# Optimization experiments

Measured on AMD Instinct MI355X. Metric: run time of the kernel, lower is better.

Reference implementation:

```python
import jax, jax.numpy as jnp
import numpy as np

NBINS = (128, 64, 32)
LOG2PI = float(np.log(2.0 * np.pi))


def _quadratic_spline_stack(x, genes_oi, local_gene_ix, delta, uh, uw):
    """Stack of piecewise-quadratic (piecewise-linear density) splines on [0,1].
    Per split with n heights / n-1 widths (n-1 bins). Returns (outputs, logabsdet)."""
    uh_oi = uh[genes_oi]  # [G, sum(n)]
    uw_oi = uw[genes_oi]  # [G, sum(n-1)]
    outputs = x
    logabsdet = jnp.zeros_like(x)
    oh = ow = od = 0
    for n in NBINS:
        nh, nw = n, n - 1
        uhs = uh_oi[:, oh:oh + nh]
        uws = uw_oi[:, ow:ow + nw]
        ds = delta[:, od:od + nh]
        oh += nh; ow += nw; od += nh
        # per-gene bin widths / locations
        widths_g = jax.nn.softmax(uws, axis=-1)                     # [G, nw]
        bl = jnp.cumsum(widths_g, axis=-1)
        bl = bl.at[:, -1].set(1.0)
        bin_loc_g = jnp.pad(bl, ((0, 0), (1, 0)))                   # [G, nw+1]
        # gather per cut
        w = widths_g[local_gene_ix]                                 # [N, nw]
        loc = bin_loc_g[local_gene_ix]                              # [N, nw+1]
        # per-cut knot heights: gene baseline + cell/gene delta, normalized to unit area
        h_un = jnp.exp(uhs[local_gene_ix] + ds)                     # [N, nh]
        area = jnp.sum(0.5 * (h_un[:, :-1] + h_un[:, 1:]) * w, axis=-1, keepdims=True)
        h = h_un / area                                             # [N, nh]
        seg = 0.5 * (h[:, :-1] + h[:, 1:]) * w                      # bin masses [N, nw]
        left_cdf = jnp.pad(jnp.cumsum(seg, axis=-1)[:, :-1], ((0, 0), (1, 0)))  # [N, nw]
        # locate bin
        bin_idx = jnp.clip(jnp.sum(outputs[:, None] >= loc, axis=-1) - 1, 0, nw - 1)
        gi = bin_idx[:, None]
        loc_l = jnp.take_along_axis(loc, gi, -1)[:, 0]
        w_b = jnp.take_along_axis(w, gi, -1)[:, 0]
        cdf_l = jnp.take_along_axis(left_cdf, gi, -1)[:, 0]
        h_l = jnp.take_along_axis(h, gi, -1)[:, 0]
        h_r = jnp.take_along_axis(h, gi + 1, -1)[:, 0]
        alpha = (outputs - loc_l) / w_b
        outputs = (0.5 * (h_r - h_l) * w_b) * alpha * alpha + h_l * w_b * alpha + cdf_l
        logabsdet = logabsdet + jnp.log(h_l + (h_r - h_l) * alpha)
    return outputs, logabsdet


def setup_inputs() -> dict:
    key = jax.random.key(0)
    ks = jax.random.split(key, 10)
    B, L, G_total, G_oi, C, N = 512, 16, 20000, 500, 224, 200000
    clustering = jax.random.uniform(ks[0], (B, L), dtype=jnp.float32)
    coordinates = jax.random.uniform(ks[1], (N,), dtype=jnp.float32, minval=1e-4, maxval=1.0 - 1e-4)
    genes_oi = jax.random.randint(ks[2], (G_oi,), 0, G_total)
    local_gene_ix = jax.random.randint(ks[3], (N,), 0, G_oi)
    local_cellxgene_ix = jax.random.randint(ks[4], (N,), 0, B * G_oi)
    localcellxgene_ix = jax.random.randint(ks[5], (N,), 0, B * G_total)
    logit_weight = jax.random.normal(ks[6], (G_total, L, C), dtype=jnp.float32) * 0.01
    rho_weight = jax.random.normal(ks[7], (G_total, L), dtype=jnp.float32) * 0.05
    rho_bias = 1e-5 + (1.0 - 1e-5) * jax.random.uniform(ks[8], (G_total,), dtype=jnp.float32)
    k9, k10 = jax.random.split(ks[9])
    unnormalized_heights = jax.random.normal(k9, (G_total, sum(NBINS)), dtype=jnp.float32) * 0.1
    unnormalized_widths = jax.random.normal(k10, (G_total, sum(n - 1 for n in NBINS)), dtype=jnp.float32) * 0.1
    return dict(clustering=clustering, coordinates=coordinates, genes_oi=genes_oi,
                local_gene_ix=local_gene_ix, local_cellxgene_ix=local_cellxgene_ix,
                localcellxgene_ix=localcellxgene_ix, logit_weight=logit_weight,
                rho_weight=rho_weight, rho_bias=rho_bias,
                unnormalized_heights=unnormalized_heights,
                unnormalized_widths=unnormalized_widths)


def reference(clustering, coordinates, genes_oi, local_gene_ix, local_cellxgene_ix,
              localcellxgene_ix, logit_weight, rho_weight, rho_bias,
              unnormalized_heights, unnormalized_widths):
    B = clustering.shape[0]
    G = genes_oi.shape[0]
    n_total_genes = rho_bias.shape[0]
    # Decoder (n_layers=0 -> nn_output = latent)
    lw_oi = logit_weight[genes_oi]                                   # [G, L, C]
    mixture_delta = jnp.einsum('bl,glc->bgc', clustering, lw_oi)     # [B, G, C]
    rho_delta = clustering @ rho_weight.T                            # [B, G_total]
    rho = jax.nn.softmax(jnp.log(rho_bias)[None, :] + rho_delta, axis=-1)
    rho_cuts = rho.reshape(-1)[localcellxgene_ix]                    # [N]
    md_cuts = mixture_delta.reshape(B * G, -1)[local_cellxgene_ix]   # [N, C]
    _, lik_mixture = _quadratic_spline_stack(coordinates, genes_oi, local_gene_ix,
                                             md_cuts, unnormalized_heights, unnormalized_widths)
    lik_overall = jnp.log(rho_cuts) + jnp.log(jnp.float32(n_total_genes))
    elbo = -jnp.sum(lik_mixture + lik_overall)
    # Normal(0, exp(log_scale=0)=1) regularization log-probs
    def normal_logpdf(v):
        return -0.5 * v * v - 0.5 * LOG2PI
    elbo = elbo - jnp.sum(normal_logpdf(lw_oi))
    elbo = elbo - jnp.sum(normal_logpdf(rho_weight[genes_oi]))
    return elbo
```

## Files before the change

### kernel.cpp

```cpp
#include <hip/hip_runtime.h>
#include <cstddef>

#define LOG2PI_F 1.8378770664093453f

__device__ __forceinline__ float wave_sum(float v) {
#pragma unroll
    for (int o = 32; o >= 1; o >>= 1) v += __shfl_xor(v, o, 64);
    return v;
}
__device__ __forceinline__ float wave_max(float v) {
#pragma unroll
    for (int o = 32; o >= 1; o >>= 1) v = fmaxf(v, __shfl_xor(v, o, 64));
    return v;
}
__device__ __forceinline__ float wave_scan_incl(float v, int lane) {
#pragma unroll
    for (int o = 1; o < 64; o <<= 1) {
        float t = __shfl_up(v, o, 64);
        if (lane >= o) v += t;
    }
    return v;
}

__global__ void k_logrb(const float* __restrict__ rho_bias, float* __restrict__ logrb, int G_total) {
    int g = blockIdx.x * blockDim.x + threadIdx.x;
    if (g < G_total) logrb[g] = __logf(rho_bias[g]);
}

__global__ void k_prep_genes(const int* __restrict__ genes_oi,
                             const float* __restrict__ uh, const float* __restrict__ uw,
                             float4* __restrict__ pk) {
    const int g = blockIdx.x;
    const int t = threadIdx.x;
    const int gs = genes_oi[g];
    const float* uhg = uh + (size_t)gs * 224;
    const float* uwg = uw + (size_t)gs * 221;
    float4* pkg = pk + (size_t)g * 224;

    const int NH[3] = {128, 64, 32};
    const int OH[3] = {0, 128, 192};
    const int OW[3] = {0, 127, 190};
    const int SO[3] = {0, 128, 191};
#pragma unroll
    for (int lev = 0; lev < 3; ++lev) {
        const int nw = NH[lev] - 1;
        float v0 = (t < nw)      ? uwg[OW[lev] + t]      : -INFINITY;
        float v1 = (t + 64 < nw) ? uwg[OW[lev] + t + 64] : -INFINITY;
        float mx = wave_max(fmaxf(v0, v1));
        float e0 = (t < nw)      ? __expf(v0 - mx) : 0.f;
        float e1 = (t + 64 < nw) ? __expf(v1 - mx) : 0.f;
        float inv = 1.0f / wave_sum(e0 + e1);
        float w0 = e0 * inv, w1 = e1 * inv;
        float i0 = wave_scan_incl(w0, t);
        float tot0 = __shfl(i0, 63, 64);
        float i1 = wave_scan_incl(w1, t) + tot0;
        if (t < nw) {
            float loc = (t == nw - 1) ? 1.0f : i0;
            pkg[SO[lev] + t] = make_float4(uhg[OH[lev] + t + 1], 0.5f * w0, loc, 0.f);
        }
        if (t + 64 < nw) {
            int j = t + 64;
            float loc = (j == nw - 1) ? 1.0f : i1;
            pkg[SO[lev] + j] = make_float4(uhg[OH[lev] + j + 1], 0.5f * w1, loc, 0.f);
        }
    }
    if (t == 0) pkg[127] = make_float4(uhg[0], uhg[128], uhg[192], 0.f);
}

__global__ void k_prep_lwT(const int* __restrict__ genes_oi,
                           const float* __restrict__ lw, const float* __restrict__ rw,
                           float* __restrict__ lwT, float* __restrict__ pB) {
    const int g = blockIdx.x;
    const int tid = threadIdx.x;
    const int gs = genes_oi[g];
    const float* src = lw + (size_t)gs * 3584;
    float* dst = lwT + (size_t)g * 3584;
    float acc = 0.f;
    if (tid < 224) {
        float vv[16];
#pragma unroll
        for (int l = 0; l < 16; ++l) {
            float v = src[l * 224 + tid];
            vv[l] = v;
            acc = fmaf(v, v, acc);
        }
        float4* d4 = (float4*)(dst + (size_t)tid * 16);
#pragma unroll
        for (int q = 0; q < 4; ++q)
            d4[q] = make_float4(vv[4 * q + 0], vv[4 * q + 1], vv[4 * q + 2], vv[4 * q + 3]);
    }
    if (tid < 16) { float v = rw[(size_t)gs * 16 + tid]; acc = fmaf(v, v, acc); }
    __shared__ float sm[256];
    sm[tid] = acc;
    __syncthreads();
    for (int o = 128; o > 0; o >>= 1) { if (tid < o) sm[tid] += sm[tid + o]; __syncthreads(); }
    if (tid == 0) pB[g] = 0.5f * sm[0] + 0.5f * LOG2PI_F * (3584.0f + 16.0f);
}

__global__ void k_lse(const float* __restrict__ clustering, const float* __restrict__ rw,
                      const float* __restrict__ logrb, float* __restrict__ lse, int G_total) {
    const int b = blockIdx.x;
    const int tid = threadIdx.x;
    __shared__ float cl_s[16];
    if (tid < 16) cl_s[tid] = clustering[(size_t)b * 16 + tid];
    __syncthreads();
    float m = -INFINITY, s = 0.f;
    for (int g = tid; g < G_total; g += blockDim.x) {
        const float4* r4 = (const float4*)(rw + (size_t)g * 16);
        float d = 0.f;
#pragma unroll
        for (int q = 0; q < 4; ++q) {
            float4 v = r4[q];
            d = fmaf(cl_s[4 * q + 0], v.x, d);
            d = fmaf(cl_s[4 * q + 1], v.y, d);
            d = fmaf(cl_s[4 * q + 2], v.z, d);
            d = fmaf(cl_s[4 * q + 3], v.w, d);
        }
        float logit = logrb[g] + d;
        float mn = fmaxf(m, logit);
        s = s * __expf(m - mn) + __expf(logit - mn);
        m = mn;
    }
    __shared__ float ms[256], ss[256];
    ms[tid] = m; ss[tid] = s;
    __syncthreads();
    for (int o = 128; o > 0; o >>= 1) {
        if (tid < o) {
            float m2 = ms[tid + o], s2 = ss[tid + o];
            float mn = fmaxf(ms[tid], m2);
            ss[tid] = ss[tid] * __expf(ms[tid] - mn) + s2 * __expf(m2 - mn);
            ms[tid] = mn;
        }
        __syncthreads();
    }
    if (tid == 0) lse[b] = ms[0] + __logf(ss[0]);
}

__global__ void k_zero(int* __restrict__ p, int n) {
    int i = blockIdx.x * blockDim.x + threadIdx.x;
    if (i < n) p[i] = 0;
}

__global__ void k_hist(const int* __restrict__ lcx, int* __restrict__ counts, int N, int G_oi) {
    int i = blockIdx.x * blockDim.x + threadIdx.x;
    if (i < N) atomicAdd(&counts[(unsigned)lcx[i] % (unsigned)G_oi], 1);
}

__global__ void k_scan(const int* __restrict__ counts, int* __restrict__ offsets,
                       int* __restrict__ cursor, int G_oi) {
    __shared__ int sm[512];
    const int t = threadIdx.x;
    int v = (t < G_oi) ? counts[t] : 0;
    sm[t] = v;
    __syncthreads();
    for (int o = 1; o < 512; o <<= 1) {
        int add = (t >= o) ? sm[t - o] : 0;
        __syncthreads();
        sm[t] += add;
        __syncthreads();
    }
    if (t < G_oi) {
        offsets[t + 1] = sm[t];
        cursor[t] = sm[t] - v;
    }
    if (t == 0) offsets[0] = 0;
}

__global__ void k_scatter(const float* __restrict__ coord, const int* __restrict__ lgix,
                          const int* __restrict__ lcx, const int* __restrict__ lc2,
                          int* __restrict__ cursor,
                          float* __restrict__ xs, int* __restrict__ b1s,
                          int* __restrict__ lc2s, int* __restrict__ ghs, int N, int G_oi) {
    int i = blockIdx.x * blockDim.x + threadIdx.x;
    if (i >= N) return;
    unsigned v = (unsigned)lcx[i];
    unsigned g = v % (unsigned)G_oi;
    int pos = atomicAdd(&cursor[g], 1);
    xs[pos]   = coord[i];
    b1s[pos]  = (int)(v / (unsigned)G_oi);
    lc2s[pos] = lc2[i];
    ghs[pos]  = lgix[i];
}

__launch_bounds__(512, 4)
__global__ void k_main2(const float* __restrict__ xs, const int* __restrict__ b1s,
                        const int* __restrict__ lc2s, const int* __restrict__ ghs,
                        const int* __restrict__ offsets,
                        const float* __restrict__ clustering,
                        const float* __restrict__ lwT,
                        const float4* __restrict__ pk,
                        const float* __restrict__ rw,
                        const float* __restrict__ logrb,
                        const float* __restrict__ lse,
                        float* __restrict__ pA, int G_oi, int G_total) {
    const int g = blockIdx.x;
    const int tid = threadIdx.x;
    const float* lwg = lwT + (size_t)g * 3584;
    const int s = offsets[g], e = offsets[g + 1];
    const float logGt = __logf((float)G_total);
    float acc = 0.f;

    for (int base = s; base < e; base += 512) {
        const int i = base + tid;
        const bool valid = i < e;
        const int isafe = valid ? i : s;
        float x = xs[isafe];
        const int b1  = b1s[isafe];
        const int lc2 = lc2s[isafe];
        const int gh  = ghs[isafe];
        const float4* pkh = pk + (size_t)gh * 224;

        float cl[16];
        {
            const float4* c4 = (const float4*)(clustering + (size_t)b1 * 16);
#pragma unroll
            for (int q = 0; q < 4; ++q) {
                float4 v = c4[q];
                cl[4 * q + 0] = v.x; cl[4 * q + 1] = v.y; cl[4 * q + 2] = v.z; cl[4 * q + 3] = v.w;
            }
        }
        const float4 uh0 = pkh[127];
        const float uh0v[3] = {uh0.x, uh0.y, uh0.z};

        float lad = 0.f;
        const int NH[3] = {128, 64, 32};
        const int OH[3] = {0, 128, 192};
        const int SO[3] = {0, 128, 191};
#pragma unroll
        for (int lev = 0; lev < 3; ++lev) {
            const int nw = NH[lev] - 1;
            const float* rowbase = lwg + (size_t)OH[lev] * 16;
            float hp;
            {
                float d = 0.f;
#pragma unroll
                for (int l = 0; l < 16; ++l) d = fmaf(cl[l], rowbase[l], d);
                hp = __expf(uh0v[lev] + d);
            }
            float h_l = hp, h_r = hp, whb = 0.f, loc_l = 0.f, cdf = 0.f, area = 0.f;
            int in = 0;
            const float4* pks = pkh + SO[lev];
            for (int j = 0; j < nw; ++j) {
                const float* row = rowbase + (size_t)(j + 1) * 16;
                float d = 0.f;
#pragma unroll
                for (int l = 0; l < 16; ++l) d = fmaf(cl[l], row[l], d);
                float4 pkv = pks[j];
                float hn = __expf(pkv.x + d);
                float seg = (hp + hn) * pkv.y;
                bool inJ = (in == j);
                if (inJ) { h_r = hn; whb = pkv.y; }
                bool adv = (x >= pkv.z) && (j < nw - 1);
                if (adv) { cdf += seg; h_l = hn; loc_l = pkv.z; in = j + 1; }
                area += seg;
                hp = hn;
            }
            float inv_area = __builtin_amdgcn_rcpf(area);
            float alpha = (x - loc_l) * 0.5f * __builtin_amdgcn_rcpf(whb);
            float t2 = whb * alpha;
            x = (t2 * fmaf(h_r - h_l, alpha, 2.f * h_l) + cdf) * inv_area;
            lad += __logf(fmaf(h_r - h_l, alpha, h_l)) - __logf(area);
        }

        unsigned b2 = (unsigned)lc2 / (unsigned)G_total;
        unsigned gt = (unsigned)lc2 - b2 * (unsigned)G_total;
        float d2 = 0.f;
        {
            const float4* c24 = (const float4*)(clustering + (size_t)b2 * 16);
            const float4* r4  = (const float4*)(rw + (size_t)gt * 16);
#pragma unroll
            for (int q = 0; q < 4; ++q) {
                float4 a = c24[q], b = r4[q];
                d2 = fmaf(a.x, b.x, d2); d2 = fmaf(a.y, b.y, d2);
                d2 = fmaf(a.z, b.z, d2); d2 = fmaf(a.w, b.w, d2);
            }
        }
        float lik = logrb[gt] + d2 - lse[b2] + logGt;
        if (valid) acc -= (lad + lik);
    }

    acc = wave_sum(acc);
    __shared__ float wsm[8];
    if ((tid & 63) == 0) wsm[tid >> 6] = acc;
    __syncthreads();
    if (tid == 0) {
        float t = 0.f;
#pragma unroll
        for (int w = 0; w < 8; ++w) t += wsm[w];
        pA[g] = t;
    }
}

__global__ void k_final(const float* __restrict__ pA, const float* __restrict__ pB,
                        float* __restrict__ out, int nA, int nB) {
    const int tid = threadIdx.x;
    float acc = 0.f;
    for (int i = tid; i < nA; i += blockDim.x) acc += pA[i];
    for (int i = tid; i < nB; i += blockDim.x) acc += pB[i];
    __shared__ float sm[256];
    sm[tid] = acc;
    __syncthreads();
    for (int o = 128; o > 0; o >>= 1) { if (tid < o) sm[tid] += sm[tid + o]; __syncthreads(); }
    if (tid == 0) out[0] = sm[0];
}

extern "C" void kernel_launch(void* const* d_in, const int* in_sizes, int n_in,
                              void* d_out, int out_size, void* d_ws, size_t ws_size,
                              hipStream_t stream) {
    const float* clustering        = (const float*)d_in[0];
    const float* coordinates       = (const float*)d_in[1];
    const int*   genes_oi          = (const int*)d_in[2];
    const int*   local_gene_ix     = (const int*)d_in[3];
    const int*   local_cellxgene_ix= (const int*)d_in[4];
    const int*   localcellxgene_ix = (const int*)d_in[5];
    const float* lw                = (const float*)d_in[6];
    const float* rw                = (const float*)d_in[7];
    const float* rho_bias          = (const float*)d_in[8];
    const float* uh                = (const float*)d_in[9];
    const float* uw                = (const float*)d_in[10];

    const int G_total = in_sizes[8];
    const int G_oi    = in_sizes[2];
    const int N       = in_sizes[1];
    const int L       = in_sizes[7] / G_total;
    const int B       = in_sizes[0] / L;

    size_t off = 0;
    char* base = (char*)d_ws;
    auto alloc = [&](size_t nbytes) {
        char* p = base + off;
        off = (off + nbytes + 15) & ~(size_t)15;
        return (void*)p;
    };
    float*  pA      = (float*)alloc(sizeof(float) * (G_oi + 16));
    float*  pB      = (float*)alloc(sizeof(float) * (G_oi + 16));
    float*  lse     = (float*)alloc(sizeof(float) * (B + 16));
    float*  logrb   = (float*)alloc(sizeof(float) * G_total);
    float*  lwT     = (float*)alloc(sizeof(float) * (size_t)G_oi * 3584);
    float4* pk      = (float4*)alloc(sizeof(float4) * (size_t)G_oi * 224);
    int*    counts  = (int*)alloc(sizeof(int) * 512);
    int*    offsets = (int*)alloc(sizeof(int) * 512);
    int*    cursor  = (int*)alloc(sizeof(int) * 512);
    float*  xs      = (float*)alloc(sizeof(float) * N);
    int*    b1s     = (int*)alloc(sizeof(int) * N);
    int*    lc2s    = (int*)alloc(sizeof(int) * N);
    int*    ghs     = (int*)alloc(sizeof(int) * N);
    (void)ws_size;

    const int TPB = 256;
    k_logrb<<<(G_total + TPB - 1) / TPB, TPB, 0, stream>>>(rho_bias, logrb, G_total);
    k_prep_genes<<<G_oi, 64, 0, stream>>>(genes_oi, uh, uw, pk);
    k_prep_lwT<<<G_oi, 256, 0, stream>>>(genes_oi, lw, rw, lwT, pB);
    k_lse<<<B, 256, 0, stream>>>(clustering, rw, logrb, lse, G_total);
    k_zero<<<2, 256, 0, stream>>>(counts, 512);
    k_hist<<<(N + TPB - 1) / TPB, TPB, 0, stream>>>(local_cellxgene_ix, counts, N, G_oi);
    k_scan<<<1, 512, 0, stream>>>(counts, offsets, cursor, G_oi);
    k_scatter<<<(N + TPB - 1) / TPB, TPB, 0, stream>>>(coordinates, local_gene_ix,
                                                       local_cellxgene_ix, localcellxgene_ix,
                                                       cursor, xs, b1s, lc2s, ghs, N, G_oi);
    k_main2<<<G_oi, 512, 0, stream>>>(xs, b1s, lc2s, ghs, offsets, clustering, lwT, pk,
                                      rw, logrb, lse, pA, G_oi, G_total);
    k_final<<<1, 256, 0, stream>>>(pA, pB, (float*)d_out, G_oi, G_oi);
}
```

Baseline: 674.8 us.

## Fuse prep kernels, stage weights in LDS, pack scatter, move rho likelihood out of main

```diff
diff --git a/kernel.cpp b/kernel.cpp
--- a/kernel.cpp
+++ b/kernel.cpp
@@ -2,6 +2,7 @@
 #include <cstddef>
 
 #define LOG2PI_F 1.8378770664093453f
+#define LOG2E_F  1.4426950408889634f
 
 __device__ __forceinline__ float wave_sum(float v) {
 #pragma unroll
@@ -22,66 +23,32 @@
     return v;
 }
 
-__global__ void k_logrb(const float* __restrict__ rho_bias, float* __restrict__ logrb, int G_total) {
-    int g = blockIdx.x * blockDim.x + threadIdx.x;
-    if (g < G_total) logrb[g] = __logf(rho_bias[g]);
-}
-
-__global__ void k_prep_genes(const int* __restrict__ genes_oi,
-                             const float* __restrict__ uh, const float* __restrict__ uw,
-                             float4* __restrict__ pk) {
-    const int g = blockIdx.x;
-    const int t = threadIdx.x;
-    const int gs = genes_oi[g];
-    const float* uhg = uh + (size_t)gs * 224;
-    const float* uwg = uw + (size_t)gs * 221;
-    float4* pkg = pk + (size_t)g * 224;
-
-    const int NH[3] = {128, 64, 32};
-    const int OH[3] = {0, 128, 192};
-    const int OW[3] = {0, 127, 190};
-    const int SO[3] = {0, 128, 191};
-#pragma unroll
-    for (int lev = 0; lev < 3; ++lev) {
-        const int nw = NH[lev] - 1;
-        float v0 = (t < nw)      ? uwg[OW[lev] + t]      : -INFINITY;
-        float v1 = (t + 64 < nw) ? uwg[OW[lev] + t + 64] : -INFINITY;
-        float mx = wave_max(fmaxf(v0, v1));
-        float e0 = (t < nw)      ? __expf(v0 - mx) : 0.f;
-        float e1 = (t + 64 < nw) ? __expf(v1 - mx) : 0.f;
-        float inv = 1.0f / wave_sum(e0 + e1);
-        float w0 = e0 * inv, w1 = e1 * inv;
-        float i0 = wave_scan_incl(w0, t);
-        float tot0 = __shfl(i0, 63, 64);
-        float i1 = wave_scan_incl(w1, t) + tot0;
-        if (t < nw) {
-            float loc = (t == nw - 1) ? 1.0f : i0;
-            pkg[SO[lev] + t] = make_float4(uhg[OH[lev] + t + 1], 0.5f * w0, loc, 0.f);
-        }
-        if (t + 64 < nw) {
-            int j = t + 64;
-            float loc = (j == nw - 1) ? 1.0f : i1;
-            pkg[SO[lev] + j] = make_float4(uhg[OH[lev] + j + 1], 0.5f * w1, loc, 0.f);
-        }
-    }
-    if (t == 0) pkg[127] = make_float4(uhg[0], uhg[128], uhg[192], 0.f);
-}
-
-__global__ void k_prep_lwT(const int* __restrict__ genes_oi,
-                           const float* __restrict__ lw, const float* __restrict__ rw,
-                           float* __restrict__ lwT, float* __restrict__ pB) {
+__global__ void k_init(const float* __restrict__ rho_bias, float* __restrict__ logrb,
+                       int* __restrict__ counts, float* __restrict__ pC, int G_total) {
+    int i = blockIdx.x * blockDim.x + threadIdx.x;
+    if (i < G_total) logrb[i] = __logf(rho_bias[i]);
+    if (i < 512) counts[i] = 0;
+    if (i == 512 + 0) pC[0] = 0.f;
+}
+
+__global__ void k_prep(const int* __restrict__ genes_oi,
+                       const float* __restrict__ uh, const float* __restrict__ uw,
+                       const float* __restrict__ lw, const float* __restrict__ rw,
+                       float4* __restrict__ pk, float* __restrict__ lwT,
+                       float* __restrict__ pB) {
     const int g = blockIdx.x;
     const int tid = threadIdx.x;
     const int gs = genes_oi[g];
-    const float* src = lw + (size_t)gs * 3584;
-    float* dst = lwT + (size_t)g * 3584;
+
     float acc = 0.f;
     if (tid < 224) {
+        const float* src = lw + (size_t)gs * 3584;
+        float* dst = lwT + (size_t)g * 3584;
         float vv[16];
 #pragma unroll
         for (int l = 0; l < 16; ++l) {
             float v = src[l * 224 + tid];
-            vv[l] = v;
+            vv[l] = v * LOG2E_F;
             acc = fmaf(v, v, acc);
         }
         float4* d4 = (float4*)(dst + (size_t)tid * 16);
@@ -90,6 +57,43 @@
             d4[q] = make_float4(vv[4 * q + 0], vv[4 * q + 1], vv[4 * q + 2], vv[4 * q + 3]);
     }
     if (tid < 16) { float v = rw[(size_t)gs * 16 + tid]; acc = fmaf(v, v, acc); }
+
+    if (tid < 64) {
+        const int t = tid;
+        const float* uhg = uh + (size_t)gs * 224;
+        const float* uwg = uw + (size_t)gs * 221;
+        float4* pkg = pk + (size_t)g * 224;
+        const int NH[3] = {128, 64, 32};
+        const int OH[3] = {0, 128, 192};
+        const int OW[3] = {0, 127, 190};
+        const int SO[3] = {0, 128, 191};
+#pragma unroll
+        for (int lev = 0; lev < 3; ++lev) {
+            const int nw = NH[lev] - 1;
+            float v0 = (t < nw)      ? uwg[OW[lev] + t]      : -INFINITY;
+            float v1 = (t + 64 < nw) ? uwg[OW[lev] + t + 64] : -INFINITY;
+            float mx = wave_max(fmaxf(v0, v1));
+            float e0 = (t < nw)      ? __expf(v0 - mx) : 0.f;
+            float e1 = (t + 64 < nw) ? __expf(v1 - mx) : 0.f;
+            float inv = 1.0f / wave_sum(e0 + e1);
+            float w0 = e0 * inv, w1 = e1 * inv;
+            float i0 = wave_scan_incl(w0, t);
+            float tot0 = __shfl(i0, 63, 64);
+            float i1 = wave_scan_incl(w1, t) + tot0;
+            if (t < nw) {
+                float loc = (t == nw - 1) ? 1.0f : i0;
+                pkg[SO[lev] + t] = make_float4(uhg[OH[lev] + t + 1] * LOG2E_F, 0.5f * w0, loc, 0.f);
+            }
+            if (t + 64 < nw) {
+                int j = t + 64;
+                float loc = (j == nw - 1) ? 1.0f : i1;
+                pkg[SO[lev] + j] = make_float4(uhg[OH[lev] + j + 1] * LOG2E_F, 0.5f * w1, loc, 0.f);
+            }
+        }
+        if (t == 0)
+            pkg[127] = make_float4(uhg[0] * LOG2E_F, uhg[128] * LOG2E_F, uhg[192] * LOG2E_F, 0.f);
+    }
+
     __shared__ float sm[256];
     sm[tid] = acc;
     __syncthreads();
@@ -136,14 +140,35 @@
     if (tid == 0) lse[b] = ms[0] + __logf(ss[0]);
 }
 
-__global__ void k_zero(int* __restrict__ p, int n) {
-    int i = blockIdx.x * blockDim.x + threadIdx.x;
-    if (i < n) p[i] = 0;
-}
-
-__global__ void k_hist(const int* __restrict__ lcx, int* __restrict__ counts, int N, int G_oi) {
-    int i = blockIdx.x * blockDim.x + threadIdx.x;
-    if (i < N) atomicAdd(&counts[(unsigned)lcx[i] % (unsigned)G_oi], 1);
+__global__ void k_histlik(const int* __restrict__ lcx, const int* __restrict__ lc2,
+                          int* __restrict__ counts,
+                          const float* __restrict__ clustering, const float* __restrict__ rw,
+                          const float* __restrict__ logrb, const float* __restrict__ lse,
+                          float* __restrict__ pC, int N, int G_oi, int G_total, float logGt) {
+    const int i = blockIdx.x * blockDim.x + threadIdx.x;
+    float acc = 0.f;
+    if (i < N) {
+        atomicAdd(&counts[(unsigned)lcx[i] % (unsigned)G_oi], 1);
+        const int v = lc2[i];
+        const unsigned b2 = (unsigned)v / (unsigned)G_total;
+        const unsigned gt = (unsigned)v - b2 * (unsigned)G_total;
+        const float4* c4 = (const float4*)(clustering + (size_t)b2 * 16);
+        const float4* r4 = (const float4*)(rw + (size_t)gt * 16);
+        float d2 = 0.f;
+#pragma unroll
+        for (int q = 0; q < 4; ++q) {
+            float4 a = c4[q], b = r4[q];
+            d2 = fmaf(a.x, b.x, d2); d2 = fmaf(a.y, b.y, d2);
+            d2 = fmaf(a.z, b.z, d2); d2 = fmaf(a.w, b.w, d2);
+        }
+        acc = -(logrb[gt] + d2 - lse[b2] + logGt);
+    }
+    acc = wave_sum(acc);
+    __shared__ float wsm[4];
+    if ((threadIdx.x & 63) == 0) wsm[threadIdx.x >> 6] = acc;
+    __syncthreads();
+    if (threadIdx.x == 0)
+        atomicAdd(pC, wsm[0] + wsm[1] + wsm[2] + wsm[3]);
 }
 
 __global__ void k_scan(const int* __restrict__ counts, int* __restrict__ offsets,
@@ -167,116 +192,104 @@
 }
 
 __global__ void k_scatter(const float* __restrict__ coord, const int* __restrict__ lgix,
-                          const int* __restrict__ lcx, const int* __restrict__ lc2,
-                          int* __restrict__ cursor,
-                          float* __restrict__ xs, int* __restrict__ b1s,
-                          int* __restrict__ lc2s, int* __restrict__ ghs, int N, int G_oi) {
+                          const int* __restrict__ lcx, int* __restrict__ cursor,
+                          int2* __restrict__ packed, int N, int G_oi) {
     int i = blockIdx.x * blockDim.x + threadIdx.x;
     if (i >= N) return;
     unsigned v = (unsigned)lcx[i];
     unsigned g = v % (unsigned)G_oi;
     int pos = atomicAdd(&cursor[g], 1);
-    xs[pos]   = coord[i];
-    b1s[pos]  = (int)(v / (unsigned)G_oi);
-    lc2s[pos] = lc2[i];
-    ghs[pos]  = lgix[i];
-}
-
-__launch_bounds__(512, 4)
-__global__ void k_main2(const float* __restrict__ xs, const int* __restrict__ b1s,
-                        const int* __restrict__ lc2s, const int* __restrict__ ghs,
+    packed[pos] = make_int2(__float_as_int(coord[i]),
+                            (int)(((v / (unsigned)G_oi) << 16) | (unsigned)lgix[i]));
+}
+
+__launch_bounds__(512)
+__global__ void k_main2(const int2* __restrict__ packed,
                         const int* __restrict__ offsets,
                         const float* __restrict__ clustering,
                         const float* __restrict__ lwT,
                         const float4* __restrict__ pk,
-                        const float* __restrict__ rw,
-                        const float* __restrict__ logrb,
-                        const float* __restrict__ lse,
-                        float* __restrict__ pA, int G_oi, int G_total) {
+                        float* __restrict__ pA, int G_oi) {
     const int g = blockIdx.x;
     const int tid = threadIdx.x;
-    const float* lwg = lwT + (size_t)g * 3584;
+    __shared__ float lds_lw[3584];
+    {
+        const float* src = lwT + (size_t)g * 3584;
+        for (int k = tid; k < 3584; k += 512) lds_lw[k] = src[k];
+    }
+    __syncthreads();
     const int s = offsets[g], e = offsets[g + 1];
-    const float logGt = __logf((float)G_total);
     float acc = 0.f;
 
     for (int base = s; base < e; base += 512) {
         const int i = base + tid;
-        const bool valid = i < e;
-        const int isafe = valid ? i : s;
-        float x = xs[isafe];
-        const int b1  = b1s[isafe];
-        const int lc2 = lc2s[isafe];
-        const int gh  = ghs[isafe];
-        const float4* pkh = pk + (size_t)gh * 224;
-
-        float cl[16];
-        {
-            const float4* c4 = (const float4*)(clustering + (size_t)b1 * 16);
-#pragma unroll
-            for (int q = 0; q < 4; ++q) {
-                float4 v = c4[q];
-                cl[4 * q + 0] = v.x; cl[4 * q + 1] = v.y; cl[4 * q + 2] = v.z; cl[4 * q + 3] = v.w;
+        if (i < e) {
+            const int2 p = packed[i];
+            float x = __int_as_float(p.x);
+            const int b1 = (int)((unsigned)p.y >> 16);
+            const int gh = p.y & 0xffff;
+            const float4* pkh = pk + (size_t)gh * 224;
+
+            float cl[16];
+            {
+                const float4* c4 = (const float4*)(clustering + (size_t)b1 * 16);
+#pragma unroll
+                for (int q = 0; q < 4; ++q) {
+                    float4 v = c4[q];
+                    cl[4 * q + 0] = v.x; cl[4 * q + 1] = v.y;
+                    cl[4 * q + 2] = v.z; cl[4 * q + 3] = v.w;
+                }
             }
-        }
-        const float4 uh0 = pkh[127];
-        const float uh0v[3] = {uh0.x, uh0.y, uh0.z};
-
-        float lad = 0.f;
-        const int NH[3] = {128, 64, 32};
-        const int OH[3] = {0, 128, 192};
-        const int SO[3] = {0, 128, 191};
-#pragma unroll
-        for (int lev = 0; lev < 3; ++lev) {
-            const int nw = NH[lev] - 1;
-            const float* rowbase = lwg + (size_t)OH[lev] * 16;
-            float hp;
-            {
-                float d = 0.f;
-#pragma unroll
-                for (int l = 0; l < 16; ++l) d = fmaf(cl[l], rowbase[l], d);
-                hp = __expf(uh0v[lev] + d);
+            const float4 uh0 = pkh[127];
+            const float uh0v[3] = {uh0.x, uh0.y, uh0.z};
+
+            float lad = 0.f;
+            const int NH[3] = {128, 64, 32};
+            const int OH[3] = {0, 128, 192};
+            const int SO[3] = {0, 128, 191};
+#pragma unroll
+            for (int lev = 0; lev < 3; ++lev) {
+                const int nw = NH[lev] - 1;
+                const float* rowbase = lds_lw + (size_t)OH[lev] * 16;
+                float hp;
+                {
+                    const float4* rq = (const float4*)rowbase;
+                    float4 r0 = rq[0], r1 = rq[1], r2 = rq[2], r3 = rq[3];
+                    float d0 = fmaf(cl[3], r0.w, fmaf(cl[2], r0.z, fmaf(cl[1], r0.y, cl[0] * r0.x)));
+                    float d1 = fmaf(cl[7], r1.w, fmaf(cl[6], r1.z, fmaf(cl[5], r1.y, cl[4] * r1.x)));
+                    float d2 = fmaf(cl[11], r2.w, fmaf(cl[10], r2.z, fmaf(cl[9], r2.y, cl[8] * r2.x)));
+                    float d3 = fmaf(cl[15], r3.w, fmaf(cl[14], r3.z, fmaf(cl[13], r3.y, cl[12] * r3.x)));
+                    hp = exp2f(uh0v[lev] + (d0 + d1) + (d2 + d3));
+                }
+                float h_l = hp, h_r = hp, whb = 0.f, loc_l = 0.f, cdf = 0.f, area = 0.f;
+                int in = 0;
+                const float4* pks = pkh + SO[lev];
+                float4 pkv = pks[0];
+                for (int j = 0; j < nw; ++j) {
+                    float4 pknext = pks[j + 1];
+                    const float4* rq = (const float4*)(rowbase + (size_t)(j + 1) * 16);
+                    float4 r0 = rq[0], r1 = rq[1], r2 = rq[2], r3 = rq[3];
+                    float d0 = fmaf(cl[3], r0.w, fmaf(cl[2], r0.z, fmaf(cl[1], r0.y, cl[0] * r0.x)));
+                    float d1 = fmaf(cl[7], r1.w, fmaf(cl[6], r1.z, fmaf(cl[5], r1.y, cl[4] * r1.x)));
+                    float d2 = fmaf(cl[11], r2.w, fmaf(cl[10], r2.z, fmaf(cl[9], r2.y, cl[8] * r2.x)));
+                    float d3 = fmaf(cl[15], r3.w, fmaf(cl[14], r3.z, fmaf(cl[13], r3.y, cl[12] * r3.x)));
+                    float hn = exp2f(pkv.x + (d0 + d1) + (d2 + d3));
+                    float seg = (hp + hn) * pkv.y;
+                    if (in == j) { h_r = hn; whb = pkv.y; }
+                    bool adv = (x >= pkv.z) && (j < nw - 1);
+                    if (adv) { cdf += seg; h_l = hn; loc_l = pkv.z; in = j + 1; }
+                    area += seg;
+                    hp = hn;
+                    pkv = pknext;
+                }
+                float inv_area = __builtin_amdgcn_rcpf(area);
+                float alpha = (x - loc_l) * 0.5f * __builtin_amdgcn_rcpf(whb);
+                float t2 = whb * alpha;
+                x = (t2 * fmaf(h_r - h_l, alpha, 2.f * h_l) + cdf) * inv_area;
+                lad += __logf(fmaf(h_r - h_l, alpha, h_l)) - __logf(area);
             }
-            float h_l = hp, h_r = hp, whb = 0.f, loc_l = 0.f, cdf = 0.f, area = 0.f;
-            int in = 0;
-            const float4* pks = pkh + SO[lev];
-            for (int j = 0; j < nw; ++j) {
-                const float* row = rowbase + (size_t)(j + 1) * 16;
-                float d = 0.f;
-#pragma unroll
-                for (int l = 0; l < 16; ++l) d = fmaf(cl[l], row[l], d);
-                float4 pkv = pks[j];
-                float hn = __expf(pkv.x + d);
-                float seg = (hp + hn) * pkv.y;
-                bool inJ = (in == j);
-                if (inJ) { h_r = hn; whb = pkv.y; }
-                bool adv = (x >= pkv.z) && (j < nw - 1);
-                if (adv) { cdf += seg; h_l = hn; loc_l = pkv.z; in = j + 1; }
-                area += seg;
-                hp = hn;
-            }
-            float inv_area = __builtin_amdgcn_rcpf(area);
-            float alpha = (x - loc_l) * 0.5f * __builtin_amdgcn_rcpf(whb);
-            float t2 = whb * alpha;
-            x = (t2 * fmaf(h_r - h_l, alpha, 2.f * h_l) + cdf) * inv_area;
-            lad += __logf(fmaf(h_r - h_l, alpha, h_l)) - __logf(area);
-        }
-
-        unsigned b2 = (unsigned)lc2 / (unsigned)G_total;
-        unsigned gt = (unsigned)lc2 - b2 * (unsigned)G_total;
-        float d2 = 0.f;
-        {
-            const float4* c24 = (const float4*)(clustering + (size_t)b2 * 16);
-            const float4* r4  = (const float4*)(rw + (size_t)gt * 16);
-#pragma unroll
-            for (int q = 0; q < 4; ++q) {
-                float4 a = c24[q], b = r4[q];
-                d2 = fmaf(a.x, b.x, d2); d2 = fmaf(a.y, b.y, d2);
-                d2 = fmaf(a.z, b.z, d2); d2 = fmaf(a.w, b.w, d2);
-            }
-        }
-        float lik = logrb[gt] + d2 - lse[b2] + logGt;
-        if (valid) acc -= (lad + lik);
+            acc -= lad;
+        }
     }
 
     acc = wave_sum(acc);
@@ -292,11 +305,12 @@
 }
 
 __global__ void k_final(const float* __restrict__ pA, const float* __restrict__ pB,
-                        float* __restrict__ out, int nA, int nB) {
+                        const float* __restrict__ pC, float* __restrict__ out, int nA, int nB) {
     const int tid = threadIdx.x;
     float acc = 0.f;
     for (int i = tid; i < nA; i += blockDim.x) acc += pA[i];
     for (int i = tid; i < nB; i += blockDim.x) acc += pB[i];
+    if (tid == 0) acc += pC[0];
     __shared__ float sm[256];
     sm[tid] = acc;
     __syncthreads();
@@ -334,6 +348,7 @@
     };
     float*  pA      = (float*)alloc(sizeof(float) * (G_oi + 16));
     float*  pB      = (float*)alloc(sizeof(float) * (G_oi + 16));
+    float*  pC      = (float*)alloc(sizeof(float) * 16);
     float*  lse     = (float*)alloc(sizeof(float) * (B + 16));
     float*  logrb   = (float*)alloc(sizeof(float) * G_total);
     float*  lwT     = (float*)alloc(sizeof(float) * (size_t)G_oi * 3584);
@@ -341,24 +356,21 @@
     int*    counts  = (int*)alloc(sizeof(int) * 512);
     int*    offsets = (int*)alloc(sizeof(int) * 512);
     int*    cursor  = (int*)alloc(sizeof(int) * 512);
-    float*  xs      = (float*)alloc(sizeof(float) * N);
-    int*    b1s     = (int*)alloc(sizeof(int) * N);
-    int*    lc2s    = (int*)alloc(sizeof(int) * N);
-    int*    ghs     = (int*)alloc(sizeof(int) * N);
+    int2*   packed  = (int2*)alloc(sizeof(int2) * (size_t)N);
     (void)ws_size;
 
+    const float logGt = logf((float)G_total);
     const int TPB = 256;
-    k_logrb<<<(G_total + TPB - 1) / TPB, TPB, 0, stream>>>(rho_bias, logrb, G_total);
-    k_prep_genes<<<G_oi, 64, 0, stream>>>(genes_oi, uh, uw, pk);
-    k_prep_lwT<<<G_oi, 256, 0, stream>>>(genes_oi, lw, rw, lwT, pB);
+
+    k_prep<<<G_oi, 256, 0, stream>>>(genes_oi, uh, uw, lw, rw, pk, lwT, pB);
+    k_init<<<(G_total + TPB - 1) / TPB, TPB, 0, stream>>>(rho_bias, logrb, counts, pC, G_total);
     k_lse<<<B, 256, 0, stream>>>(clustering, rw, logrb, lse, G_total);
-    k_zero<<<2, 256, 0, stream>>>(counts, 512);
-    k_hist<<<(N + TPB - 1) / TPB, TPB, 0, stream>>>(local_cellxgene_ix, counts, N, G_oi);
+    k_histlik<<<(N + TPB - 1) / TPB, TPB, 0, stream>>>(local_cellxgene_ix, localcellxgene_ix,
+                                                       counts, clustering, rw, logrb, lse,
+                                                       pC, N, G_oi, G_total, logGt);
     k_scan<<<1, 512, 0, stream>>>(counts, offsets, cursor, G_oi);
     k_scatter<<<(N + TPB - 1) / TPB, TPB, 0, stream>>>(coordinates, local_gene_ix,
-                                                       local_cellxgene_ix, localcellxgene_ix,
-                                                       cursor, xs, b1s, lc2s, ghs, N, G_oi);
-    k_main2<<<G_oi, 512, 0, stream>>>(xs, b1s, lc2s, ghs, offsets, clustering, lwT, pk,
-                                      rw, logrb, lse, pA, G_oi, G_total);
-    k_final<<<1, 256, 0, stream>>>(pA, pB, (float*)d_out, G_oi, G_oi);
-}
+                                                       local_cellxgene_ix, cursor, packed, N, G_oi);
+    k_main2<<<G_oi, 512, 0, stream>>>(packed, offsets, clustering, lwT, pk, pA, G_oi);
+    k_final<<<1, 256, 0, stream>>>(pA, pB, pC, (float*)d_out, G_oi, G_oi);
+}
```

Measured after the change: 699.3 us. +3.6%, slower.
